# Kernel optimization log

Measured on AMD Instinct MI355X. Metric: run time of the kernel, lower is better.

The kernel has to match this reference:

```python
import jax, jax.numpy as jnp
import numpy as np

RADIUS = 8
NUM = 200
EPS = 1e-8


def _conv2d(x, k, pad_mode):
    # x: [B,1,H,W], k: [kh,kw]; same-size conv with given numpy-style padding mode
    ph, pw = k.shape[0] // 2, k.shape[1] // 2
    xp = jnp.pad(x, ((0, 0), (0, 0), (ph, ph), (pw, pw)), mode=pad_mode)
    return jax.lax.conv_general_dilated(
        xp, k[None, None], (1, 1), 'VALID',
        dimension_numbers=('NCHW', 'OIHW', 'NCHW'))


def _gauss_kernel7():
    xs = np.arange(7, dtype=np.float32) - 3.0
    g = np.exp(-0.5 * xs ** 2)
    g /= g.sum()
    return jnp.asarray(np.outer(g, g))


def get_corners(imgs):
    B, _, H, W = imgs.shape
    # kornia rgb_to_grayscale
    gray = 0.299 * imgs[:, 0:1] + 0.587 * imgs[:, 1:2] + 0.114 * imgs[:, 2:3]
    # kornia CornerGFTT: sobel gradients (normalized), gaussian-smoothed structure tensor, min eigenvalue
    sob = jnp.array([[-1., 0., 1.], [-2., 0., 2.], [-1., 0., 1.]], jnp.float32) / 8.0
    dx = _conv2d(gray, sob, 'edge')
    dy = _conv2d(gray, sob.T, 'edge')
    g = _gauss_kernel7()
    dx2 = _conv2d(dx * dx, g, 'reflect')
    dy2 = _conv2d(dy * dy, g, 'reflect')
    dxy = _conv2d(dx * dy, g, 'reflect')
    tr = dx2 + dy2
    det = dx2 * dy2 - dxy * dxy
    resp = 0.5 * (tr - jnp.sqrt(jnp.abs(tr * tr - 4.0 * det)))  # GFTT score (min eigval)
    # kornia nms2d with 5x5 window: keep local maxima
    mp = jax.lax.reduce_window(resp, -jnp.inf, jax.lax.max,
                               (1, 1, 5, 5), (1, 1, 1, 1),
                               [(0, 0), (0, 0), (2, 2), (2, 2)])
    resp = jnp.where(resp == mp, resp, 0.0)
    # unfold/mask/fold with kernel=stride=RADIUS == per non-overlapping 8x8 block:
    # keep elements equal to the block max and > 0
    r = RADIUS
    blk = resp.reshape(B, 1, H // r, r, W // r, r)
    bmax = blk.max(axis=(3, 5), keepdims=True)
    blk = jnp.where((blk > 0) & (blk == bmax), blk, 0.0)
    corners = blk.reshape(B, H * W)
    # top-200 scatter then binarize
    vals, idx = jax.lax.top_k(corners, NUM)
    out = jnp.zeros_like(corners).at[jnp.arange(B)[:, None], idx].set(vals)
    return (out > 0).astype(imgs.dtype).reshape(B, 1, H, W)


def setup_inputs() -> dict:
    key = jax.random.key(0)
    k1, k2, k3, k4 = jax.random.split(key, 4)
    B, N, D, H, W = 16, 2048, 256, 384, 384
    return {
        'descriptors': jax.random.normal(k1, (B, N, D), jnp.float32),
        'scores': jax.random.uniform(k2, (B, N), jnp.float32),
        'scores_dense': jax.random.normal(k3, (B, 1, H, W), jnp.float32),
        'imgs': jax.random.uniform(k4, (B, 3, H, W), jnp.float32),
    }


def reference(descriptors, scores, scores_dense, imgs):
    corners = get_corners(imgs)
    # all-pairs cosine similarity within each batch: pcos[b,i,j]
    norms = jnp.linalg.norm(descriptors, axis=-1)  # [B,N]
    dots = jnp.einsum('bnd,bmd->bnm', descriptors, descriptors)
    pcos = dots / jnp.maximum(norms[:, :, None] * norms[:, None, :], EPS)
    # BCEWithLogitsLoss(scores_dense, corners), mean reduction
    bce = jnp.mean(jnp.logaddexp(0.0, scores_dense) - scores_dense * corners)
    return bce + jnp.mean(jax.nn.relu(pcos))
```

## Files before the change

### kernel.cpp

```cpp
#include <hip/hip_runtime.h>

#define H 384
#define W 384
#define HWSZ (H * W)
#define NB 16
#define ND 2048
#define DD 256

#define OFF_RESP  256
#define OFF_CVAL  9437440
#define OFF_CPOS  9584896
#define OFF_DESCB 9732352
#define OFF_INV   26509568
#define OFF_PSOFT 26640640
#define OFF_PGEMM 26643200
#define OFF_PCORN 26652160

__device__ __forceinline__ int clampi(int v) { return v < 0 ? 0 : (v > 383 ? 383 : v); }
__device__ __forceinline__ int refl(int v) { return v < 0 ? -v : (v >= 384 ? 766 - v : v); }

__device__ __forceinline__ unsigned f2e4m3(float x) {
  float a = fabsf(x);
  unsigned s = (__float_as_uint(x) >> 31) << 7;
  if (a >= 448.f) return s | 0x7E;
  if (a < 0.015625f) {
    int m = (int)rintf(a * 512.f);
    return s | (unsigned)m;
  }
  unsigned u = __float_as_uint(a);
  u += 0x7FFFF + ((u >> 20) & 1);
  unsigned e = (u >> 23) - 120;
  unsigned m = (u >> 20) & 7;
  return s | (e << 3) | m;
}

typedef float f32x4 __attribute__((ext_vector_type(4)));

__device__ __forceinline__ void load_lds16(const void* g, void* l) {
  __builtin_amdgcn_global_load_lds((const __attribute__((address_space(1))) void*)g,
                                   (__attribute__((address_space(3))) void*)l, 16, 0, 0);
}

__global__ __launch_bounds__(256) void stage1_kernel(const float* __restrict__ imgs,
                                                     float* __restrict__ resp,
                                                     const float* __restrict__ desc,
                                                     unsigned char* __restrict__ descF8,
                                                     float* __restrict__ invn) {
  __shared__ float pbuf[4448];
  __shared__ float ubuf[3648];
  float* p0 = pbuf;
  float* p1 = pbuf + 1482;
  float* p2 = pbuf + 2964;
  float* glf = ubuf;
  float* t0 = ubuf;
  float* t1 = ubuf + 1216;
  float* t2 = ubuf + 2432;

  if (blockIdx.x >= 2304) {
    int wave = threadIdx.x >> 6, lane = threadIdx.x & 63;
    int row = (blockIdx.x - 2304) * 4 + wave;
    const float4* src = (const float4*)(desc + (size_t)row * DD);
    float4 v = src[lane];
    unsigned pk = f2e4m3(v.x) | (f2e4m3(v.y) << 8) | (f2e4m3(v.z) << 16) | (f2e4m3(v.w) << 24);
    ((unsigned*)(descF8 + (size_t)row * DD))[lane] = pk;
    float ss = v.x * v.x + v.y * v.y + v.z * v.z + v.w * v.w;
    for (int off = 32; off; off >>= 1) ss += __shfl_down(ss, off, 64);
    if (lane == 0) invn[row] = 1.f / fmaxf(sqrtf(ss), 1e-4f);
    return;
  }

  const float GW[7] = {0.0044330482f, 0.0540055826f, 0.2420362294f, 0.3990502160f,
                       0.2420362294f, 0.0540055826f, 0.0044330482f};
  int bid = blockIdx.x;
  int b = bid / 144;
  int t = bid % 144;
  int Y0 = (t / 12) * 32, X0 = (t % 12) * 32;
  const float* ib = imgs + (size_t)b * 3 * HWSZ;

  for (int i = threadIdx.x; i < 1600; i += 256) {
    int r = i / 40, c = i % 40;
    int gy = clampi(Y0 - 4 + r), gx = clampi(X0 - 4 + c);
    const float* p = ib + gy * W + gx;
    glf[r * 41 + c] = 0.299f * p[0] + 0.587f * p[HWSZ] + 0.114f * p[2 * HWSZ];
  }
  __syncthreads();

  bool interior = (X0 >= 32 && X0 <= 320 && Y0 >= 32 && Y0 <= 320);

  if (interior) {
    for (int i = threadIdx.x; i < 1444; i += 256) {
      int r = i / 38, c = i % 38;
      const float* g0 = glf + r * 41 + c;
      float a = g0[0],  bb = g0[1],  cc = g0[2];
      float d = g0[41],              e = g0[43];
      float f = g0[82], g = g0[83],  h = g0[84];
      float dx = 0.125f * ((cc - a) + 2.f * (e - d) + (h - f));
      float dy = 0.125f * ((f - a) + 2.f * (g - bb) + (h - cc));
      p0[r * 39 + c] = dx * dx;
      p1[r * 39 + c] = dy * dy;
      p2[r * 39 + c] = dx * dy;
    }
  } else {
    for (int i = threadIdx.x; i < 1444; i += 256) {
      int r = i / 38, c = i % 38;
      int py = refl(Y0 - 3 + r), px = refl(X0 - 3 + c);
      int ym = clampi(py - 1) - (Y0 - 4), y0 = py - (Y0 - 4), yp = clampi(py + 1) - (Y0 - 4);
      int xm = clampi(px - 1) - (X0 - 4), x0 = px - (X0 - 4), xp = clampi(px + 1) - (X0 - 4);
      float a = glf[ym * 41 + xm], bb = glf[ym * 41 + x0], cc = glf[ym * 41 + xp];
      float d = glf[y0 * 41 + xm], e = glf[y0 * 41 + xp];
      float f = glf[yp * 41 + xm], g = glf[yp * 41 + x0], h = glf[yp * 41 + xp];
      float dx = 0.125f * ((cc - a) + 2.f * (e - d) + (h - f));
      float dy = 0.125f * ((f - a) + 2.f * (g - bb) + (h - cc));
      p0[r * 39 + c] = dx * dx;
      p1[r * 39 + c] = dy * dy;
      p2[r * 39 + c] = dx * dy;
    }
  }
  __syncthreads();

  for (int g = threadIdx.x; g < 304; g += 256) {
    int r = g >> 3, c0 = (g & 7) * 4;
    {
      float a[10];
#pragma unroll
      for (int dc = 0; dc < 10; dc++) a[dc] = p0[r * 39 + c0 + dc];
#pragma unroll
      for (int k = 0; k < 4; k++) {
        float sv = 0.f;
#pragma unroll
        for (int j = 0; j < 7; j++) sv += GW[j] * a[k + j];
        t0[r * 32 + c0 + k] = sv;
      }
    }
    {
      float a[10];
#pragma unroll
      for (int dc = 0; dc < 10; dc++) a[dc] = p1[r * 39 + c0 + dc];
#pragma unroll
      for (int k = 0; k < 4; k++) {
        float sv = 0.f;
#pragma unroll
        for (int j = 0; j < 7; j++) sv += GW[j] * a[k + j];
        t1[r * 32 + c0 + k] = sv;
      }
    }
    {
      float a[10];
#pragma unroll
      for (int dc = 0; dc < 10; dc++) a[dc] = p2[r * 39 + c0 + dc];
#pragma unroll
      for (int k = 0; k < 4; k++) {
        float sv = 0.f;
#pragma unroll
        for (int j = 0; j < 7; j++) sv += GW[j] * a[k + j];
        t2[r * 32 + c0 + k] = sv;
      }
    }
  }
  __syncthreads();

  {
    int r0 = (threadIdx.x >> 5) * 4, c = threadIdx.x & 31;
    float s0[4], s1[4], s2[4];
    {
      float a[10];
#pragma unroll
      for (int dr = 0; dr < 10; dr++) a[dr] = t0[(r0 + dr) * 32 + c];
#pragma unroll
      for (int k = 0; k < 4; k++) {
        float sv = 0.f;
#pragma unroll
        for (int j = 0; j < 7; j++) sv += GW[j] * a[k + j];
        s0[k] = sv;
      }
    }
    {
      float a[10];
#pragma unroll
      for (int dr = 0; dr < 10; dr++) a[dr] = t1[(r0 + dr) * 32 + c];
#pragma unroll
      for (int k = 0; k < 4; k++) {
        float sv = 0.f;
#pragma unroll
        for (int j = 0; j < 7; j++) sv += GW[j] * a[k + j];
        s1[k] = sv;
      }
    }
    {
      float a[10];
#pragma unroll
      for (int dr = 0; dr < 10; dr++) a[dr] = t2[(r0 + dr) * 32 + c];
#pragma unroll
      for (int k = 0; k < 4; k++) {
        float sv = 0.f;
#pragma unroll
        for (int j = 0; j < 7; j++) sv += GW[j] * a[k + j];
        s2[k] = sv;
      }
    }
#pragma unroll
    for (int k = 0; k < 4; k++) {
      float tr = s0[k] + s1[k];
      float det = s0[k] * s1[k] - s2[k] * s2[k];
      float disc = tr * tr - 4.f * det;
      float rv = 0.5f * (tr - sqrtf(fabsf(disc)));
      resp[(size_t)b * HWSZ + (Y0 + r0 + k) * W + (X0 + c)] = rv;
    }
  }
}

__global__ __launch_bounds__(256) void stage2_kernel(const float* __restrict__ resp,
                                                     float* __restrict__ cval,
                                                     unsigned* __restrict__ cpos,
                                                     const float4* __restrict__ sd4,
                                                     float* __restrict__ psoft) {
  __shared__ float rl[68][69];
  __shared__ float rmx[68][65];
  __shared__ float r4[4];

  if (blockIdx.x >= 576) {
    int sb = blockIdx.x - 576;
    float s = 0.f;
    int base = sb * 256 + threadIdx.x;
#pragma unroll
    for (int it = 0; it < 4; it++) {
      float4 v = sd4[base + it * 147456];
      s += fmaxf(v.x, 0.f) + log1pf(expf(-fabsf(v.x))) +
           fmaxf(v.y, 0.f) + log1pf(expf(-fabsf(v.y))) +
           fmaxf(v.z, 0.f) + log1pf(expf(-fabsf(v.z))) +
           fmaxf(v.w, 0.f) + log1pf(expf(-fabsf(v.w)));
    }
    for (int off = 32; off; off >>= 1) s += __shfl_down(s, off, 64);
    if ((threadIdx.x & 63) == 0) r4[threadIdx.x >> 6] = s;
    __syncthreads();
    if (threadIdx.x == 0) psoft[sb] = r4[0] + r4[1] + r4[2] + r4[3];
    return;
  }

  int bid = blockIdx.x;
  int b = bid / 36;
  int t = bid % 36;
  int Y0 = (t / 6) * 64, X0 = (t % 6) * 64;
  const float* rb = resp + (size_t)b * HWSZ;

  for (int i = threadIdx.x; i < 68 * 68; i += 256) {
    int r = i / 68, c = i % 68;
    int gy = Y0 - 2 + r, gx = X0 - 2 + c;
    float v = -INFINITY;
    if (gy >= 0 && gy < H && gx >= 0 && gx < W) v = rb[gy * W + gx];
    rl[r][c] = v;
  }
  __syncthreads();

  for (int i = threadIdx.x; i < 68 * 64; i += 256) {
    int r = i / 64, c = i % 64;
    float m = rl[r][c];
    m = fmaxf(m, rl[r][c + 1]);
    m = fmaxf(m, rl[r][c + 2]);
    m = fmaxf(m, rl[r][c + 3]);
    m = fmaxf(m, rl[r][c + 4]);
    rmx[r][c] = m;
  }
  __syncthreads();

  for (int i = threadIdx.x; i < 4096; i += 256) {
    int r = i / 64, c = i % 64;
    float m = rmx[r][c];
    m = fmaxf(m, rmx[r + 1][c]);
    m = fmaxf(m, rmx[r + 2][c]);
    m = fmaxf(m, rmx[r + 3][c]);
    m = fmaxf(m, rmx[r + 4][c]);
    float v = rl[r + 2][c + 2];
    rl[r + 2][c + 2] = (v == m) ? v : 0.f;
  }
  __syncthreads();

  if (threadIdx.x < 64) {
    int bi = threadIdx.x / 8, bj = threadIdx.x % 8;
    float bv = 0.f;
    unsigned bp = 0;
    for (int rr = 0; rr < 8; rr++)
      for (int cc = 0; cc < 8; cc++) {
        float v = rl[bi * 8 + rr + 2][bj * 8 + cc + 2];
        if (v > bv) { bv = v; bp = (unsigned)((Y0 + bi * 8 + rr) * W + (X0 + bj * 8 + cc)); }
      }
    int ci = b * 2304 + (Y0 / 8 + bi) * 48 + (X0 / 8 + bj);
    cval[ci] = bv;
    cpos[ci] = bp;
  }
}

__global__ __launch_bounds__(256) void stage3_kernel(const float* __restrict__ cval,
                                                     const unsigned* __restrict__ cpos,
                                                     const float* __restrict__ sd,
                                                     float* __restrict__ pcorn,
                                                     const unsigned char* __restrict__ descF8,
                                                     const float* __restrict__ invn,
                                                     float* __restrict__ pgemm) {
  __shared__ char lA[128 * 128];
  __shared__ char lB[128 * 128];
  __shared__ float r4[4];
  __shared__ int hist[256];
  __shared__ int pick[2];
  __shared__ unsigned eqpos[256];
  __shared__ int eqcnt;
  __shared__ int ri[4];

  if (blockIdx.x < 16) {
    int b = blockIdx.x;
    int t = threadIdx.x;
    int lane = t & 63;

    unsigned bits[9], pos[9];
#pragma unroll
    for (int q = 0; q < 9; q++) {
      int i = t + q * 256;
      unsigned vb = 0, p = 0;
      if (i < 2304) {
        float v = cval[b * 2304 + i];
        if (v > 0.f) { vb = __float_as_uint(v); p = cpos[b * 2304 + i]; }
      }
      bits[q] = vb; pos[q] = p;
    }

    int P = 0;
#pragma unroll
    for (int q = 0; q < 9; q++) P += (bits[q] != 0u);
    for (int off = 32; off; off >>= 1) P += __shfl_down(P, off, 64);
    if (lane == 0) ri[t >> 6] = P;
    __syncthreads();
    int Ptot = ri[0] + ri[1] + ri[2] + ri[3];
    if (Ptot == 0) { if (t == 0) pcorn[b] = 0.f; return; }
    int K = Ptot < 200 ? Ptot : 200;

    unsigned prefix = 0;
    int krem = K;
    for (int shift = 24; shift >= 0; shift -= 8) {
      hist[t] = 0;
      __syncthreads();
#pragma unroll
      for (int q = 0; q < 9; q++) {
        if (bits[q] != 0u &&
            (shift == 24 || (bits[q] >> (shift + 8)) == (prefix >> (shift + 8))))
          atomicAdd(&hist[(bits[q] >> shift) & 0xFF], 1);
      }
      __syncthreads();
      if (t < 64) {
        int h0 = hist[4 * t], h1 = hist[4 * t + 1], h2 = hist[4 * t + 2], h3 = hist[4 * t + 3];
        int tot = h0 + h1 + h2 + h3;
        int acc = tot;
        for (int d = 1; d < 64; d <<= 1) {
          int o = __shfl_down(acc, d, 64);
          if (t + d < 64) acc += o;
        }
        int excl = acc - tot;
        int G3 = excl, G2 = excl + h3, G1 = excl + h3 + h2, G0 = excl + h3 + h2 + h1;
        if (G0 < krem && G0 + h0 >= krem) { pick[0] = 4 * t;     pick[1] = G0; }
        if (G1 < krem && G1 + h1 >= krem) { pick[0] = 4 * t + 1; pick[1] = G1; }
        if (G2 < krem && G2 + h2 >= krem) { pick[0] = 4 * t + 2; pick[1] = G2; }
        if (G3 < krem && G3 + h3 >= krem) { pick[0] = 4 * t + 3; pick[1] = G3; }
      }
      __syncthreads();
      prefix |= ((unsigned)pick[0]) << shift;
      krem -= pick[1];
      __syncthreads();
    }

    if (t == 0) eqcnt = 0;
    __syncthreads();
    float s = 0.f;
#pragma unroll
    for (int q = 0; q < 9; q++) {
      if (bits[q] > prefix) s += sd[(size_t)b * HWSZ + pos[q]];
      else if (bits[q] != 0u && bits[q] == prefix) {
        int idx = atomicAdd(&eqcnt, 1);
        if (idx < 256) eqpos[idx] = pos[q];
      }
    }
    __syncthreads();
    int m = eqcnt;
    if (m <= krem) {
      if (t < m) s += sd[(size_t)b * HWSZ + eqpos[t]];
    } else {
      int mm = m < 256 ? m : 256;
      if (t < mm) {
        unsigned p = eqpos[t];
        int rank = 0;
        for (int u = 0; u < mm; u++) rank += (eqpos[u] < p);
        if (rank < krem) s += sd[(size_t)b * HWSZ + p];
      }
    }
    for (int off = 32; off; off >>= 1) s += __shfl_down(s, off, 64);
    if (lane == 0) r4[t >> 6] = s;
    __syncthreads();
    if (t == 0) pcorn[b] = r4[0] + r4[1] + r4[2] + r4[3];
    return;
  }

  int bxl = blockIdx.x - 16;
  int bx = ((bxl & 7) * 272) + (bxl >> 3);
  int batch = bx / 136;
  int rem = bx % 136;
  int ti = 0, rowlen = 16;
  while (rem >= rowlen) { rem -= rowlen; rowlen--; ti++; }
  int tj = ti + rem;

  const unsigned char* Ab = descF8 + (size_t)batch * ND * DD;
  const float* inv = invn + batch * ND;
  int I0 = ti * 128, J0 = tj * 128;

  int tid = threadIdx.x;
  int wave = tid >> 6, lane = tid & 63;
  int rm = lane & 15, kq = lane >> 4;
  int wr = wave >> 1, wc = wave & 1;
  int lrow = lane >> 3;
  int lcolb = ((lane & 7) ^ lrow) << 4;
  int cx = rm & 7;

  f32x4 accf[4][4];
#pragma unroll
  for (int m = 0; m < 4; m++)
#pragma unroll
    for (int n = 0; n < 4; n++) accf[m][n] = (f32x4){0.f, 0.f, 0.f, 0.f};

  for (int k0 = 0; k0 < DD; k0 += 128) {
#pragma unroll
    for (int q = 0; q < 4; q++) {
      int chunk = wave * 4 + q;
      load_lds16(Ab + (size_t)(I0 + chunk * 8 + lrow) * DD + k0 + lcolb, lA + chunk * 1024);
      load_lds16(Ab + (size_t)(J0 + chunk * 8 + lrow) * DD + k0 + lcolb, lB + chunk * 1024);
    }
    __syncthreads();
#pragma unroll
    for (int kk = 0; kk < 128; kk += 32) {
      long af[4], bfr[4];
      int koff = kk + kq * 8;
      int pcol = ((((koff >> 4) ^ cx) << 4) | (koff & 8));
#pragma unroll
      for (int m = 0; m < 4; m++)
        af[m] = *reinterpret_cast<const long*>(lA + (wr * 64 + m * 16 + rm) * 128 + pcol);
#pragma unroll
      for (int n = 0; n < 4; n++)
        bfr[n] = *reinterpret_cast<const long*>(lB + (wc * 64 + n * 16 + rm) * 128 + pcol);
#pragma unroll
      for (int m = 0; m < 4; m++)
#pragma unroll
        for (int n = 0; n < 4; n++)
          accf[m][n] = __builtin_amdgcn_mfma_f32_16x16x32_fp8_fp8(af[m], bfr[n], accf[m][n], 0, 0, 0);
    }
    __syncthreads();
  }

  float wgt = (ti == tj) ? 1.f : 2.f;
  float invC[4];
#pragma unroll
  for (int n = 0; n < 4; n++) invC[n] = inv[J0 + wc * 64 + n * 16 + rm];
  float psum = 0.f;
#pragma unroll
  for (int m = 0; m < 4; m++) {
#pragma unroll
    for (int r = 0; r < 4; r++) {
      float invR = inv[I0 + wr * 64 + m * 16 + kq * 4 + r];
#pragma unroll
      for (int n = 0; n < 4; n++) psum += fmaxf(accf[m][n][r] * invR * invC[n], 0.f);
    }
  }
  psum *= wgt;
  for (int off = 32; off; off >>= 1) psum += __shfl_down(psum, off, 64);
  if (lane == 0) r4[wave] = psum;
  __syncthreads();
  if (tid == 0) pgemm[bx] = r4[0] + r4[1] + r4[2] + r4[3];
}

__global__ __launch_bounds__(256) void finalize_kernel(const float* __restrict__ psoft,
                                                       const float* __restrict__ pcorn,
                                                       const float* __restrict__ pgemm,
                                                       float* __restrict__ out) {
  __shared__ float r4[4];
  float bce = 0.f;
  for (int i = threadIdx.x; i < 576; i += 256) bce += psoft[i];
  if (threadIdx.x < 16) bce -= pcorn[threadIdx.x];
  float g = 0.f;
  for (int i = threadIdx.x; i < 2176; i += 256) g += pgemm[i];
  float t = bce * (1.f / 2359296.f) + g * (1.f / 67108864.f);
  for (int off = 32; off; off >>= 1) t += __shfl_down(t, off, 64);
  if ((threadIdx.x & 63) == 0) r4[threadIdx.x >> 6] = t;
  __syncthreads();
  if (threadIdx.x == 0) out[0] = r4[0] + r4[1] + r4[2] + r4[3];
}

extern "C" void kernel_launch(void* const* d_in, const int* in_sizes, int n_in,
                              void* d_out, int out_size, void* d_ws, size_t ws_size,
                              hipStream_t stream) {
  (void)in_sizes; (void)n_in; (void)out_size; (void)ws_size;
  const float* desc = (const float*)d_in[0];
  const float* sd = (const float*)d_in[2];
  const float* imgs = (const float*)d_in[3];
  float* out = (float*)d_out;

  char* w = (char*)d_ws;
  float* resp = (float*)(w + OFF_RESP);
  float* cval = (float*)(w + OFF_CVAL);
  unsigned* cpos = (unsigned*)(w + OFF_CPOS);
  unsigned char* descF8 = (unsigned char*)(w + OFF_DESCB);
  float* invn = (float*)(w + OFF_INV);
  float* psoft = (float*)(w + OFF_PSOFT);
  float* pgemm = (float*)(w + OFF_PGEMM);
  float* pcorn = (float*)(w + OFF_PCORN);

  stage1_kernel<<<10496, 256, 0, stream>>>(imgs, resp, desc, descF8, invn);
  stage2_kernel<<<1152, 256, 0, stream>>>(resp, cval, cpos, (const float4*)sd, psoft);
  stage3_kernel<<<2192, 256, 0, stream>>>(cval, cpos, sd, pcorn, descF8, invn, pgemm);
  finalize_kernel<<<1, 256, 0, stream>>>(psoft, pcorn, pgemm, out);
}
```

Measured before the change: 155.8 us.

## Merge NMS, softplus, top-k and GEMM into one kernel with spin-wait counters

Stage2 and stage3 become a single launch. The first 16 blocks (top-k per batch) spin on per-batch atomic counters, which the NMS blocks increment once their block-max results are written. NMS tiles shrink to 64x32 so there are more blocks, and the softplus and GEMM blocks fill the rest of the grid. This removes one kernel launch and the grid-wide barrier between the stages, so the GEMM can overlap with NMS. In exchange it relies on the waiting blocks not starving the producer blocks, since the spin-waiters sit at the lowest block indices and are scheduled first.

Result: slower. 247.2 us (+58.7%).

```diff
diff --git a/kernel.cpp b/kernel.cpp
--- a/kernel.cpp
+++ b/kernel.cpp
@@ -15,6 +15,7 @@
 #define OFF_PSOFT 26640640
 #define OFF_PGEMM 26643200
 #define OFF_PCORN 26652160
+#define OFF_NMSCNT 26652288
 
 __device__ __forceinline__ int clampi(int v) { return v < 0 ? 0 : (v > 383 ? 383 : v); }
 __device__ __forceinline__ int refl(int v) { return v < 0 ? -v : (v >= 384 ? 766 - v : v); }
@@ -45,7 +46,8 @@
                                                      float* __restrict__ resp,
                                                      const float* __restrict__ desc,
                                                      unsigned char* __restrict__ descF8,
-                                                     float* __restrict__ invn) {
+                                                     float* __restrict__ invn,
+                                                     int* __restrict__ nmsCnt) {
   __shared__ float pbuf[4448];
   __shared__ float ubuf[3648];
   float* p0 = pbuf;
@@ -57,6 +59,7 @@
   float* t2 = ubuf + 2432;
 
   if (blockIdx.x >= 2304) {
+    if (blockIdx.x == 2304 && threadIdx.x < 16) nmsCnt[threadIdx.x] = 0;
     int wave = threadIdx.x >> 6, lane = threadIdx.x & 63;
     int row = (blockIdx.x - 2304) * 4 + wave;
     const float4* src = (const float4*)(desc + (size_t)row * DD);
@@ -212,115 +215,44 @@
 __global__ __launch_bounds__(256) void stage2_kernel(const float* __restrict__ resp,
                                                      float* __restrict__ cval,
                                                      unsigned* __restrict__ cpos,
-                                                     const float4* __restrict__ sd4,
-                                                     float* __restrict__ psoft) {
-  __shared__ float rl[68][69];
-  __shared__ float rmx[68][65];
-  __shared__ float r4[4];
-
-  if (blockIdx.x >= 576) {
-    int sb = blockIdx.x - 576;
-    float s = 0.f;
-    int base = sb * 256 + threadIdx.x;
-#pragma unroll
-    for (int it = 0; it < 4; it++) {
-      float4 v = sd4[base + it * 147456];
-      s += fmaxf(v.x, 0.f) + log1pf(expf(-fabsf(v.x))) +
-           fmaxf(v.y, 0.f) + log1pf(expf(-fabsf(v.y))) +
-           fmaxf(v.z, 0.f) + log1pf(expf(-fabsf(v.z))) +
-           fmaxf(v.w, 0.f) + log1pf(expf(-fabsf(v.w)));
-    }
-    for (int off = 32; off; off >>= 1) s += __shfl_down(s, off, 64);
-    if ((threadIdx.x & 63) == 0) r4[threadIdx.x >> 6] = s;
-    __syncthreads();
-    if (threadIdx.x == 0) psoft[sb] = r4[0] + r4[1] + r4[2] + r4[3];
-    return;
-  }
-
-  int bid = blockIdx.x;
-  int b = bid / 36;
-  int t = bid % 36;
-  int Y0 = (t / 6) * 64, X0 = (t % 6) * 64;
-  const float* rb = resp + (size_t)b * HWSZ;
-
-  for (int i = threadIdx.x; i < 68 * 68; i += 256) {
-    int r = i / 68, c = i % 68;
-    int gy = Y0 - 2 + r, gx = X0 - 2 + c;
-    float v = -INFINITY;
-    if (gy >= 0 && gy < H && gx >= 0 && gx < W) v = rb[gy * W + gx];
-    rl[r][c] = v;
-  }
-  __syncthreads();
-
-  for (int i = threadIdx.x; i < 68 * 64; i += 256) {
-    int r = i / 64, c = i % 64;
-    float m = rl[r][c];
-    m = fmaxf(m, rl[r][c + 1]);
-    m = fmaxf(m, rl[r][c + 2]);
-    m = fmaxf(m, rl[r][c + 3]);
-    m = fmaxf(m, rl[r][c + 4]);
-    rmx[r][c] = m;
-  }
-  __syncthreads();
-
-  for (int i = threadIdx.x; i < 4096; i += 256) {
-    int r = i / 64, c = i % 64;
-    float m = rmx[r][c];
-    m = fmaxf(m, rmx[r + 1][c]);
-    m = fmaxf(m, rmx[r + 2][c]);
-    m = fmaxf(m, rmx[r + 3][c]);
-    m = fmaxf(m, rmx[r + 4][c]);
-    float v = rl[r + 2][c + 2];
-    rl[r + 2][c + 2] = (v == m) ? v : 0.f;
-  }
-  __syncthreads();
-
-  if (threadIdx.x < 64) {
-    int bi = threadIdx.x / 8, bj = threadIdx.x % 8;
-    float bv = 0.f;
-    unsigned bp = 0;
-    for (int rr = 0; rr < 8; rr++)
-      for (int cc = 0; cc < 8; cc++) {
-        float v = rl[bi * 8 + rr + 2][bj * 8 + cc + 2];
-        if (v > bv) { bv = v; bp = (unsigned)((Y0 + bi * 8 + rr) * W + (X0 + bj * 8 + cc)); }
-      }
-    int ci = b * 2304 + (Y0 / 8 + bi) * 48 + (X0 / 8 + bj);
-    cval[ci] = bv;
-    cpos[ci] = bp;
-  }
-}
-
-__global__ __launch_bounds__(256) void stage3_kernel(const float* __restrict__ cval,
-                                                     const unsigned* __restrict__ cpos,
                                                      const float* __restrict__ sd,
-                                                     float* __restrict__ pcorn,
+                                                     float* __restrict__ psoft,
                                                      const unsigned char* __restrict__ descF8,
                                                      const float* __restrict__ invn,
-                                                     float* __restrict__ pgemm) {
-  __shared__ char lA[128 * 128];
-  __shared__ char lB[128 * 128];
-  __shared__ float r4[4];
-  __shared__ int hist[256];
-  __shared__ int pick[2];
-  __shared__ unsigned eqpos[256];
-  __shared__ int eqcnt;
-  __shared__ int ri[4];
+                                                     float* __restrict__ pgemm,
+                                                     float* __restrict__ pcorn,
+                                                     int* __restrict__ nmsCnt) {
+  alignas(16) __shared__ char smem[32768];
+  int tid = threadIdx.x;
 
   if (blockIdx.x < 16) {
+    int* hist = (int*)smem;
+    int* pick = (int*)(smem + 1024);
+    int* eqcnt = (int*)(smem + 1032);
+    int* ri = (int*)(smem + 1040);
+    unsigned* eqpos = (unsigned*)(smem + 1056);
+    float* r4 = (float*)(smem + 2080);
+
     int b = blockIdx.x;
-    int t = threadIdx.x;
+    int t = tid;
     int lane = t & 63;
+
+    if (t == 0) {
+      while (__hip_atomic_load(&nmsCnt[b], __ATOMIC_RELAXED, __HIP_MEMORY_SCOPE_AGENT) < 72)
+        __builtin_amdgcn_s_sleep(8);
+      __threadfence();
+    }
+    __syncthreads();
 
     unsigned bits[9], pos[9];
 #pragma unroll
     for (int q = 0; q < 9; q++) {
       int i = t + q * 256;
-      unsigned vb = 0, p = 0;
-      if (i < 2304) {
-        float v = cval[b * 2304 + i];
-        if (v > 0.f) { vb = __float_as_uint(v); p = cpos[b * 2304 + i]; }
-      }
-      bits[q] = vb; pos[q] = p;
+      float v = __hip_atomic_load(&cval[b * 2304 + i], __ATOMIC_RELAXED, __HIP_MEMORY_SCOPE_AGENT);
+      unsigned p = __hip_atomic_load(&cpos[b * 2304 + i], __ATOMIC_RELAXED, __HIP_MEMORY_SCOPE_AGENT);
+      unsigned vb = 0, pp = 0;
+      if (v > 0.f) { vb = __float_as_uint(v); pp = p; }
+      bits[q] = vb; pos[q] = pp;
     }
 
     int P = 0;
@@ -366,19 +298,19 @@
       __syncthreads();
     }
 
-    if (t == 0) eqcnt = 0;
+    if (t == 0) *eqcnt = 0;
     __syncthreads();
     float s = 0.f;
 #pragma unroll
     for (int q = 0; q < 9; q++) {
       if (bits[q] > prefix) s += sd[(size_t)b * HWSZ + pos[q]];
       else if (bits[q] != 0u && bits[q] == prefix) {
-        int idx = atomicAdd(&eqcnt, 1);
+        int idx = atomicAdd(eqcnt, 1);
         if (idx < 256) eqpos[idx] = pos[q];
       }
     }
     __syncthreads();
-    int m = eqcnt;
+    int m = *eqcnt;
     if (m <= krem) {
       if (t < m) s += sd[(size_t)b * HWSZ + eqpos[t]];
     } else {
@@ -397,7 +329,92 @@
     return;
   }
 
-  int bxl = blockIdx.x - 16;
+  if (blockIdx.x < 1168) {
+    float (*rl)[37] = (float (*)[37])smem;
+    float (*rmx)[32] = (float (*)[32])(smem + 10080);
+
+    int bid = blockIdx.x - 16;
+    int b = bid / 72;
+    int t = bid % 72;
+    int Y0 = (t / 12) * 64, X0 = (t % 12) * 32;
+    const float* rb = resp + (size_t)b * HWSZ;
+
+    for (int i = tid; i < 68 * 36; i += 256) {
+      int r = i / 36, c = i % 36;
+      int gy = Y0 - 2 + r, gx = X0 - 2 + c;
+      float v = -INFINITY;
+      if (gy >= 0 && gy < H && gx >= 0 && gx < W) v = rb[gy * W + gx];
+      rl[r][c] = v;
+    }
+    __syncthreads();
+
+    for (int i = tid; i < 68 * 32; i += 256) {
+      int r = i / 32, c = i % 32;
+      float m = rl[r][c];
+      m = fmaxf(m, rl[r][c + 1]);
+      m = fmaxf(m, rl[r][c + 2]);
+      m = fmaxf(m, rl[r][c + 3]);
+      m = fmaxf(m, rl[r][c + 4]);
+      rmx[r][c] = m;
+    }
+    __syncthreads();
+
+    for (int i = tid; i < 2048; i += 256) {
+      int r = i / 32, c = i % 32;
+      float m = rmx[r][c];
+      m = fmaxf(m, rmx[r + 1][c]);
+      m = fmaxf(m, rmx[r + 2][c]);
+      m = fmaxf(m, rmx[r + 3][c]);
+      m = fmaxf(m, rmx[r + 4][c]);
+      float v = rl[r + 2][c + 2];
+      rl[r + 2][c + 2] = (v == m) ? v : 0.f;
+    }
+    __syncthreads();
+
+    if (tid < 32) {
+      int bi = tid >> 2, bj = tid & 3;
+      float bv = 0.f;
+      unsigned bp = 0;
+      for (int rr = 0; rr < 8; rr++)
+        for (int cc = 0; cc < 8; cc++) {
+          float v = rl[bi * 8 + rr + 2][bj * 8 + cc + 2];
+          if (v > bv) { bv = v; bp = (unsigned)((Y0 + bi * 8 + rr) * W + (X0 + bj * 8 + cc)); }
+        }
+      int ci = b * 2304 + (Y0 / 8 + bi) * 48 + (X0 / 8 + bj);
+      __hip_atomic_store(&cval[ci], bv, __ATOMIC_RELAXED, __HIP_MEMORY_SCOPE_AGENT);
+      __hip_atomic_store(&cpos[ci], bp, __ATOMIC_RELAXED, __HIP_MEMORY_SCOPE_AGENT);
+    }
+    __threadfence();
+    __syncthreads();
+    if (tid == 0) atomicAdd(&nmsCnt[b], 1);
+    return;
+  }
+
+  if (blockIdx.x < 1744) {
+    int sb = blockIdx.x - 1168;
+    float* r4 = (float*)smem;
+    const float4* sd4 = (const float4*)sd;
+    float s = 0.f;
+    int base = sb * 256 + tid;
+#pragma unroll
+    for (int it = 0; it < 4; it++) {
+      float4 v = sd4[base + it * 147456];
+      s += fmaxf(v.x, 0.f) + log1pf(expf(-fabsf(v.x))) +
+           fmaxf(v.y, 0.f) + log1pf(expf(-fabsf(v.y))) +
+           fmaxf(v.z, 0.f) + log1pf(expf(-fabsf(v.z))) +
+           fmaxf(v.w, 0.f) + log1pf(expf(-fabsf(v.w)));
+    }
+    for (int off = 32; off; off >>= 1) s += __shfl_down(s, off, 64);
+    if ((tid & 63) == 0) r4[tid >> 6] = s;
+    __syncthreads();
+    if (tid == 0) psoft[sb] = r4[0] + r4[1] + r4[2] + r4[3];
+    return;
+  }
+
+  char* lA = smem;
+  char* lB = smem + 16384;
+
+  int bxl = blockIdx.x - 1744;
   int bx = ((bxl & 7) * 272) + (bxl >> 3);
   int batch = bx / 136;
   int rem = bx % 136;
@@ -409,7 +426,6 @@
   const float* inv = invn + batch * ND;
   int I0 = ti * 128, J0 = tj * 128;
 
-  int tid = threadIdx.x;
   int wave = tid >> 6, lane = tid & 63;
   int rm = lane & 15, kq = lane >> 4;
   int wr = wave >> 1, wc = wave & 1;
@@ -467,6 +483,7 @@
   }
   psum *= wgt;
   for (int off = 32; off; off >>= 1) psum += __shfl_down(psum, off, 64);
+  float* r4 = (float*)smem;
   if (lane == 0) r4[wave] = psum;
   __syncthreads();
   if (tid == 0) pgemm[bx] = r4[0] + r4[1] + r4[2] + r4[3];
@@ -507,9 +524,10 @@
   float* psoft = (float*)(w + OFF_PSOFT);
   float* pgemm = (float*)(w + OFF_PGEMM);
   float* pcorn = (float*)(w + OFF_PCORN);
-
-  stage1_kernel<<<10496, 256, 0, stream>>>(imgs, resp, desc, descF8, invn);
-  stage2_kernel<<<1152, 256, 0, stream>>>(resp, cval, cpos, (const float4*)sd, psoft);
-  stage3_kernel<<<2192, 256, 0, stream>>>(cval, cpos, sd, pcorn, descF8, invn, pgemm);
+  int* nmsCnt = (int*)(w + OFF_NMSCNT);
+
+  stage1_kernel<<<10496, 256, 0, stream>>>(imgs, resp, desc, descF8, invn, nmsCnt);
+  stage2_kernel<<<3920, 256, 0, stream>>>(resp, cval, cpos, sd, psoft,
+                                          descF8, invn, pgemm, pcorn, nmsCnt);
   finalize_kernel<<<1, 256, 0, stream>>>(psoft, pcorn, pgemm, out);
 }
```
